# Kernel optimization log

Hardware: AMD Instinct MI355X
Metric: run time of the kernel (lower is better)

The kernel has to match this reference:

```python
import jax, jax.numpy as jnp
import numpy as np

XI_DIM = 4
LENS = jnp.array([0.5, 0.5, 1.0], dtype=jnp.float32)
NOISE_SCALE = jnp.array([0.01, 0.01], dtype=jnp.float32)
PRIOR_SCALE = jnp.array([0.25, 0.5, 0.5, 0.5], dtype=jnp.float32)
LOG2PI = float(np.log(2.0 * np.pi))
_TRIL_R, _TRIL_C = np.tril_indices(XI_DIM, k=-1)  # strict lower triangle (6 entries)


def _mlp(y, W1, b1, W2, b2, W3, b3):
    h = jax.nn.relu(y @ W1 + b1)
    h = jax.nn.relu(h @ W2 + b2)
    return h @ W3 + b3


def _forward_D(xi):
    # robot-arm forward kinematics; xi: [..., 4] -> end point D: [..., 2]
    a1 = xi[..., 1]
    a2 = a1 + xi[..., 2]
    a3 = a2 + xi[..., 3]
    px = LENS[0] * jnp.cos(a1) + LENS[1] * jnp.cos(a2) + LENS[2] * jnp.cos(a3)
    py = xi[..., 0] + LENS[0] * jnp.sin(a1) + LENS[1] * jnp.sin(a2) + LENS[2] * jnp.sin(a3)
    return jnp.stack([px, py], axis=-1)


def setup_inputs() -> dict:
    key = jax.random.key(0)
    N, P = 524288, 8
    ks = jax.random.split(key, 24)
    # observed data exactly as observed_data(): xi ~ Normal(0, prior_scale), y = f(xi)['D'] + noise
    xi_data = jax.random.normal(ks[0], (N, XI_DIM), dtype=jnp.float32) * PRIOR_SCALE
    y = _forward_D(xi_data) + NOISE_SCALE * jax.random.normal(ks[1], (N, 2), dtype=jnp.float32)
    zs = jax.random.normal(ks[2], (N, P, XI_DIM), dtype=jnp.float32)
    inp = {"y": y, "zs": zs}
    base = [("W1", (2, 20)), ("b1", (20,)), ("W2", (20, 10)), ("b2", (10,))]
    i = 3
    for pre, out_dim in (("mu", XI_DIM), ("ld", XI_DIM), ("lo", XI_DIM * (XI_DIM + 1) // 2 - XI_DIM)):
        for nm, sh in base + [("W3", (10, out_dim)), ("b3", (out_dim,))]:
            inp[f"{pre}_{nm}"] = jax.random.normal(ks[i], sh, dtype=jnp.float32) * 0.3
            i += 1
    return inp


def reference(y, zs,
              mu_W1, mu_b1, mu_W2, mu_b2, mu_W3, mu_b3,
              ld_W1, ld_b1, ld_W2, ld_b2, ld_W3, ld_b3,
              lo_W1, lo_b1, lo_W2, lo_b2, lo_W3, lo_b3):
    N, P, D = zs.shape
    q_mu = _mlp(y, mu_W1, mu_b1, mu_W2, mu_b2, mu_W3, mu_b3)                  # [N, 4]
    q_L_diag = jax.nn.softplus(_mlp(y, ld_W1, ld_b1, ld_W2, ld_b2, ld_W3, ld_b3))  # [N, 4]
    q_L_off = _mlp(y, lo_W1, lo_b1, lo_W2, lo_b2, lo_W3, lo_b3)               # [N, 6]
    # batched Cholesky factors L: [N, 4, 4]
    L = jnp.zeros((N, D, D), dtype=y.dtype)
    L = L.at[:, _TRIL_R, _TRIL_C].set(q_L_off)
    di = jnp.arange(D)
    L = L.at[:, di, di].set(q_L_diag)
    # reparameterized samples: xi = mu + L @ z, vectorized over (N, P)
    xi = q_mu[:, None, :] + jnp.einsum('nij,npj->npi', L, zs)                 # [N, P, 4]
    # prior log-prob (independent Normal(0, prior_scale)), summed over dims
    log_prior = jnp.sum(-0.5 * (xi / PRIOR_SCALE) ** 2 - jnp.log(PRIOR_SCALE) - 0.5 * LOG2PI, axis=-1)
    # likelihood: Normal(f(xi)['D'], noise_scale).log_prob(y), summed over y_dim
    Dpt = _forward_D(xi)                                                      # [N, P, 2]
    r = (y[:, None, :] - Dpt) / NOISE_SCALE
    log_lik = jnp.sum(-0.5 * r ** 2 - jnp.log(NOISE_SCALE) - 0.5 * LOG2PI, axis=-1)
    datafit = jnp.mean(log_prior + log_lik, axis=1)                           # [N]
    # MVN entropy with scale_tril L: 0.5*d*(1+log 2pi) + sum log diag(L)
    entropy = 0.5 * D * (1.0 + LOG2PI) + jnp.sum(jnp.log(q_L_diag), axis=-1)
    return jnp.mean(datafit + entropy)
```

## Files before the change

kernel.cpp:

```cpp
#include <hip/hip_runtime.h>
#include <math.h>

#define C_ALL 12.838199208f

typedef float v2 __attribute__((ext_vector_type(2)));
static __device__ __forceinline__ v2 splat(float s) { return (v2){s, s}; }
#define FMA2 __builtin_elementwise_fma
#define MAX2 __builtin_elementwise_max

struct WPtrs { const float* p[18]; };

__device__ __forceinline__ float softplus_f(float x) {
    return fmaxf(x, 0.0f) + __logf(1.0f + __expf(-fabsf(x)));
}
__device__ __forceinline__ v2 sp2(v2 x) {
    v2 r; r.x = softplus_f(x.x); r.y = softplus_f(x.y); return r;
}

template <int OD>
__device__ __forceinline__ void mlp4(const float* __restrict__ W1,
                                     const float* __restrict__ b1,
                                     const float* __restrict__ W2,
                                     const float* __restrict__ b2,
                                     const float* __restrict__ W3,
                                     const float* __restrict__ b3,
                                     v2 Y0a, v2 Y1a, v2 Y0b, v2 Y1b,
                                     v2* oa, v2* ob) {
    v2 h2a[10], h2b[10];
#pragma unroll
    for (int k = 0; k < 10; ++k) { const v2 bb = splat(b2[k]); h2a[k] = bb; h2b[k] = bb; }
#pragma unroll
    for (int j = 0; j < 20; ++j) {
        const float w0 = W1[j], w1 = W1[20 + j], bb = b1[j];
        const v2 h1a = MAX2(FMA2(Y0a, splat(w0), FMA2(Y1a, splat(w1), splat(bb))), splat(0.0f));
        const v2 h1b = MAX2(FMA2(Y0b, splat(w0), FMA2(Y1b, splat(w1), splat(bb))), splat(0.0f));
#pragma unroll
        for (int k = 0; k < 10; ++k) {
            const v2 w = splat(W2[j * 10 + k]);
            h2a[k] = FMA2(h1a, w, h2a[k]);
            h2b[k] = FMA2(h1b, w, h2b[k]);
        }
    }
#pragma unroll
    for (int k = 0; k < 10; ++k) { h2a[k] = MAX2(h2a[k], splat(0.0f)); h2b[k] = MAX2(h2b[k], splat(0.0f)); }
#pragma unroll
    for (int d = 0; d < OD; ++d) { const v2 bb = splat(b3[d]); oa[d] = bb; ob[d] = bb; }
#pragma unroll
    for (int k = 0; k < 10; ++k) {
#pragma unroll
        for (int d = 0; d < OD; ++d) {
            const v2 w = splat(W3[k * OD + d]);
            oa[d] = FMA2(h2a[k], w, oa[d]);
            ob[d] = FMA2(h2b[k], w, ob[d]);
        }
    }
}

template <int OD>
__device__ __forceinline__ void mlp1(const float* __restrict__ W1, const float* __restrict__ b1,
                                     const float* __restrict__ W2, const float* __restrict__ b2,
                                     const float* __restrict__ W3, const float* __restrict__ b3,
                                     float y0, float y1, float* out) {
    float h2[10];
#pragma unroll
    for (int k = 0; k < 10; ++k) h2[k] = b2[k];
#pragma unroll
    for (int j = 0; j < 20; ++j) {
        const float h1 = fmaxf(0.0f, fmaf(y0, W1[j], fmaf(y1, W1[20 + j], b1[j])));
#pragma unroll
        for (int k = 0; k < 10; ++k) h2[k] = fmaf(h1, W2[j * 10 + k], h2[k]);
    }
#pragma unroll
    for (int k = 0; k < 10; ++k) h2[k] = fmaxf(0.0f, h2[k]);
#pragma unroll
    for (int d = 0; d < OD; ++d) out[d] = b3[d];
#pragma unroll
    for (int k = 0; k < 10; ++k)
#pragma unroll
        for (int d = 0; d < OD; ++d) out[d] = fmaf(h2[k], W3[k * OD + d], out[d]);
}

__device__ __forceinline__ void store_params(float* __restrict__ pr, int row,
                                             float m0, float m1, float m2, float m3,
                                             float d0, float d1, float d2, float d3,
                                             float L10, float L20, float L21,
                                             float L30, float L31, float L32) {
    float4* q = reinterpret_cast<float4*>(pr + (size_t)row * 16);
    q[0] = make_float4(m0, m1, m2, m3);
    q[1] = make_float4(d0, d1, d2, d3);
    q[2] = make_float4(L10, L20, L21, L30);
    q[3] = make_float4(L31, L32, __logf(d0 * d1 * d2 * d3), 0.0f);
}

__global__ __launch_bounds__(256) void avi_params(
    const float* __restrict__ y, WPtrs wp, float* __restrict__ pr, int N) {
    const int tid = threadIdx.x;
    const int r0 = blockIdx.x * 1024 + tid;

    if (r0 + 768 < N) {
        const float2 ya = *reinterpret_cast<const float2*>(y + 2 * (size_t)(r0));
        const float2 yb = *reinterpret_cast<const float2*>(y + 2 * (size_t)(r0 + 256));
        const float2 yc = *reinterpret_cast<const float2*>(y + 2 * (size_t)(r0 + 512));
        const float2 yd = *reinterpret_cast<const float2*>(y + 2 * (size_t)(r0 + 768));
        const v2 Y0a = {ya.x, yb.x}, Y1a = {ya.y, yb.y};
        const v2 Y0b = {yc.x, yd.x}, Y1b = {yc.y, yd.y};

        v2 mua[4], mub[4], lda[4], ldb[4], loa[6], lob[6];
        mlp4<4>(wp.p[0], wp.p[1], wp.p[2], wp.p[3], wp.p[4], wp.p[5],
                Y0a, Y1a, Y0b, Y1b, mua, mub);
        mlp4<4>(wp.p[6], wp.p[7], wp.p[8], wp.p[9], wp.p[10], wp.p[11],
                Y0a, Y1a, Y0b, Y1b, lda, ldb);
        mlp4<6>(wp.p[12], wp.p[13], wp.p[14], wp.p[15], wp.p[16], wp.p[17],
                Y0a, Y1a, Y0b, Y1b, loa, lob);

        const v2 da0 = sp2(lda[0]), da1 = sp2(lda[1]), da2 = sp2(lda[2]), da3 = sp2(lda[3]);
        const v2 db0 = sp2(ldb[0]), db1 = sp2(ldb[1]), db2 = sp2(ldb[2]), db3 = sp2(ldb[3]);

        store_params(pr, r0,       mua[0].x, mua[1].x, mua[2].x, mua[3].x,
                     da0.x, da1.x, da2.x, da3.x,
                     loa[0].x, loa[1].x, loa[2].x, loa[3].x, loa[4].x, loa[5].x);
        store_params(pr, r0 + 256, mua[0].y, mua[1].y, mua[2].y, mua[3].y,
                     da0.y, da1.y, da2.y, da3.y,
                     loa[0].y, loa[1].y, loa[2].y, loa[3].y, loa[4].y, loa[5].y);
        store_params(pr, r0 + 512, mub[0].x, mub[1].x, mub[2].x, mub[3].x,
                     db0.x, db1.x, db2.x, db3.x,
                     lob[0].x, lob[1].x, lob[2].x, lob[3].x, lob[4].x, lob[5].x);
        store_params(pr, r0 + 768, mub[0].y, mub[1].y, mub[2].y, mub[3].y,
                     db0.y, db1.y, db2.y, db3.y,
                     lob[0].y, lob[1].y, lob[2].y, lob[3].y, lob[4].y, lob[5].y);
    } else {
        for (int s = 0; s < 4; ++s) {
            const int row = r0 + s * 256;
            if (row >= N) continue;
            const float2 yv = *reinterpret_cast<const float2*>(y + 2 * (size_t)row);
            float mu[4], ld[4], lo[6];
            mlp1<4>(wp.p[0], wp.p[1], wp.p[2], wp.p[3], wp.p[4], wp.p[5], yv.x, yv.y, mu);
            mlp1<4>(wp.p[6], wp.p[7], wp.p[8], wp.p[9], wp.p[10], wp.p[11], yv.x, yv.y, ld);
            mlp1<6>(wp.p[12], wp.p[13], wp.p[14], wp.p[15], wp.p[16], wp.p[17], yv.x, yv.y, lo);
            store_params(pr, row, mu[0], mu[1], mu[2], mu[3],
                         softplus_f(ld[0]), softplus_f(ld[1]), softplus_f(ld[2]), softplus_f(ld[3]),
                         lo[0], lo[1], lo[2], lo[3], lo[4], lo[5]);
        }
    }
}

__global__ __launch_bounds__(256) void avi_tail(
    const float* __restrict__ y, const float* __restrict__ zs,
    const float* __restrict__ pr, float* __restrict__ out, int N, float invN) {
    __shared__ float wsum[4];
    const int tid = threadIdx.x;
    const int n = blockIdx.x * 256 + tid;
    float rv = 0.0f;
    if (n < N) {
        const float4* pq = reinterpret_cast<const float4*>(pr + (size_t)n * 16);
        const float4 p0 = pq[0], p1 = pq[1], p2 = pq[2], p3 = pq[3];
        const float2 yv = *reinterpret_cast<const float2*>(y + 2 * (size_t)n);
        const float y0 = yv.x, y1 = yv.y;

        const float4* zp = reinterpret_cast<const float4*>(zs + (size_t)n * 32);
        float4 z[8];
#pragma unroll
        for (int p = 0; p < 8; ++p) z[p] = zp[p];
        __builtin_amdgcn_sched_barrier(0);

        const float m0 = p0.x, m1 = p0.y, m2 = p0.z, m3 = p0.w;
        const float d0 = p1.x, d1 = p1.y, d2 = p1.z, d3 = p1.w;
        const float L10 = p2.x, L20 = p2.y, L21 = p2.z, L30 = p2.w;
        const float L31 = p3.x, L32 = p3.y, slog = p3.z;

        float acc = 0.0f;
#pragma unroll
        for (int p = 0; p < 8; ++p) {
            const float xi0 = fmaf(d0, z[p].x, m0);
            const float xi1 = fmaf(d1, z[p].y, fmaf(L10, z[p].x, m1));
            const float xi2 = fmaf(d2, z[p].z, fmaf(L21, z[p].y, fmaf(L20, z[p].x, m2)));
            const float xi3 = fmaf(d3, z[p].w, fmaf(L32, z[p].z, fmaf(L31, z[p].y, fmaf(L30, z[p].x, m3))));

            const float a1 = xi1, a2 = xi1 + xi2, a3 = a2 + xi3;
            float s1, c1, s2, c2, s3, c3;
            __sincosf(a1, &s1, &c1);
            __sincosf(a2, &s2, &c2);
            __sincosf(a3, &s3, &c3);
            const float px = fmaf(0.5f, c1, fmaf(0.5f, c2, c3));
            const float py = xi0 + fmaf(0.5f, s1, fmaf(0.5f, s2, s3));

            const float q0 = xi0 * 4.0f, q1 = xi1 * 2.0f, q2 = xi2 * 2.0f, q3 = xi3 * 2.0f;
            const float pq2 = fmaf(q0, q0, fmaf(q1, q1, fmaf(q2, q2, q3 * q3)));
            const float r0 = (y0 - px) * 100.0f;
            const float r1 = (y1 - py) * 100.0f;
            acc = fmaf(-0.5f, pq2 + fmaf(r0, r0, r1 * r1), acc);
        }
        rv = fmaf(0.125f, acc, C_ALL + slog);
    }

#pragma unroll
    for (int d = 32; d > 0; d >>= 1) rv += __shfl_down(rv, d);
    if ((tid & 63) == 0) wsum[tid >> 6] = rv;
    __syncthreads();
    if (tid == 0) {
        const float s = wsum[0] + wsum[1] + wsum[2] + wsum[3];
        atomicAdd(out, s * invN);
    }
}

extern "C" void kernel_launch(void* const* d_in, const int* in_sizes, int n_in,
                              void* d_out, int out_size, void* d_ws, size_t ws_size,
                              hipStream_t stream) {
    const float* y = (const float*)d_in[0];
    const float* zs = (const float*)d_in[1];
    WPtrs wp;
    for (int i = 0; i < 18; ++i) wp.p[i] = (const float*)d_in[2 + i];
    float* out = (float*)d_out;
    float* pr = (float*)d_ws;
    const int N = in_sizes[0] / 2;

    hipMemsetAsync(out, 0, sizeof(float), stream);
    avi_params<<<(N + 1023) / 1024, 256, 0, stream>>>(y, wp, pr, N);
    avi_tail<<<(N + 255) / 256, 256, 0, stream>>>(y, zs, pr, out, N, 1.0f / (float)N);
}
```

Before: 183.5 us.

## Fuse param MLP and tail into one kernel, prefetching zs during MLP

Merges the parameter-MLP kernel and the sampling/likelihood tail kernel into a single kernel. Each thread now handles 4 rows and keeps the MLP outputs in registers instead of writing a 64-byte-per-row parameter buffer to workspace and reading it back. Half of the zs loads are issued before the MLP so their latency overlaps that compute, and the tail math is packed into 2-wide vector ops. The cost is much higher register pressure from holding 64 floats of z plus MLP state, with launch_bounds(256,2) limiting occupancy, and only N/1024 blocks in the grid.

```diff
diff --git a/kernel.cpp b/kernel.cpp
--- a/kernel.cpp
+++ b/kernel.cpp
@@ -56,6 +56,48 @@
     }
 }
 
+__device__ __forceinline__ v2 tail_pack(const v2* mu, v2 d0, v2 d1, v2 d2, v2 d3,
+                                        const v2* lo, v2 Y0, v2 Y1,
+                                        const float4* z1, const float4* z2) {
+    const v2 L10 = lo[0], L20 = lo[1], L21 = lo[2];
+    const v2 L30 = lo[3], L31 = lo[4], L32 = lo[5];
+    v2 acc = splat(0.0f);
+#pragma unroll
+    for (int p = 0; p < 8; ++p) {
+        const v2 zx = {z1[p].x, z2[p].x}, zy = {z1[p].y, z2[p].y};
+        const v2 zz = {z1[p].z, z2[p].z}, zw = {z1[p].w, z2[p].w};
+
+        const v2 xi0 = FMA2(d0, zx, mu[0]);
+        const v2 xi1 = FMA2(d1, zy, FMA2(L10, zx, mu[1]));
+        const v2 xi2 = FMA2(d2, zz, FMA2(L21, zy, FMA2(L20, zx, mu[2])));
+        const v2 xi3 = FMA2(d3, zw, FMA2(L32, zz, FMA2(L31, zy, FMA2(L30, zx, mu[3]))));
+
+        const v2 a1 = xi1, a2 = xi1 + xi2, a3 = a2 + xi3;
+        float s1x, c1x, s1y, c1y, s2x, c2x, s2y, c2y, s3x, c3x, s3y, c3y;
+        __sincosf(a1.x, &s1x, &c1x);
+        __sincosf(a1.y, &s1y, &c1y);
+        __sincosf(a2.x, &s2x, &c2x);
+        __sincosf(a2.y, &s2y, &c2y);
+        __sincosf(a3.x, &s3x, &c3x);
+        __sincosf(a3.y, &s3y, &c3y);
+        const v2 s1 = {s1x, s1y}, c1 = {c1x, c1y};
+        const v2 s2 = {s2x, s2y}, c2 = {c2x, c2y};
+        const v2 s3 = {s3x, s3y}, c3 = {c3x, c3y};
+
+        const v2 half = splat(0.5f);
+        const v2 px = FMA2(half, c1, FMA2(half, c2, c3));
+        const v2 py = xi0 + FMA2(half, s1, FMA2(half, s2, s3));
+
+        const v2 q0 = xi0 * splat(4.0f), q1 = xi1 * splat(2.0f);
+        const v2 q2 = xi2 * splat(2.0f), q3 = xi3 * splat(2.0f);
+        const v2 pq = FMA2(q0, q0, FMA2(q1, q1, FMA2(q2, q2, q3 * q3)));
+        const v2 r0 = (Y0 - px) * splat(100.0f);
+        const v2 r1 = (Y1 - py) * splat(100.0f);
+        acc = FMA2(splat(-0.5f), pq + FMA2(r0, r0, r1 * r1), acc);
+    }
+    return acc;
+}
+
 template <int OD>
 __device__ __forceinline__ void mlp1(const float* __restrict__ W1, const float* __restrict__ b1,
                                      const float* __restrict__ W2, const float* __restrict__ b2,
@@ -80,30 +122,62 @@
         for (int d = 0; d < OD; ++d) out[d] = fmaf(h2[k], W3[k * OD + d], out[d]);
 }
 
-__device__ __forceinline__ void store_params(float* __restrict__ pr, int row,
-                                             float m0, float m1, float m2, float m3,
-                                             float d0, float d1, float d2, float d3,
-                                             float L10, float L20, float L21,
-                                             float L30, float L31, float L32) {
-    float4* q = reinterpret_cast<float4*>(pr + (size_t)row * 16);
-    q[0] = make_float4(m0, m1, m2, m3);
-    q[1] = make_float4(d0, d1, d2, d3);
-    q[2] = make_float4(L10, L20, L21, L30);
-    q[3] = make_float4(L31, L32, __logf(d0 * d1 * d2 * d3), 0.0f);
-}
-
-__global__ __launch_bounds__(256) void avi_params(
-    const float* __restrict__ y, WPtrs wp, float* __restrict__ pr, int N) {
+__device__ float row_scalar(const float* __restrict__ y, const float* __restrict__ zs,
+                            const WPtrs& wp, int n) {
+    const float2 yv = *reinterpret_cast<const float2*>(y + 2 * (size_t)n);
+    const float y0 = yv.x, y1 = yv.y;
+    float mu[4], ld[4], lo[6];
+    mlp1<4>(wp.p[0], wp.p[1], wp.p[2], wp.p[3], wp.p[4], wp.p[5], y0, y1, mu);
+    mlp1<4>(wp.p[6], wp.p[7], wp.p[8], wp.p[9], wp.p[10], wp.p[11], y0, y1, ld);
+    mlp1<6>(wp.p[12], wp.p[13], wp.p[14], wp.p[15], wp.p[16], wp.p[17], y0, y1, lo);
+    const float d0 = softplus_f(ld[0]), d1 = softplus_f(ld[1]);
+    const float d2 = softplus_f(ld[2]), d3 = softplus_f(ld[3]);
+    const float slog = __logf(d0 * d1 * d2 * d3);
+    const float4* zp = reinterpret_cast<const float4*>(zs + (size_t)n * 32);
+    float acc = 0.0f;
+    for (int p = 0; p < 8; ++p) {
+        const float4 z = zp[p];
+        const float xi0 = fmaf(d0, z.x, mu[0]);
+        const float xi1 = fmaf(d1, z.y, fmaf(lo[0], z.x, mu[1]));
+        const float xi2 = fmaf(d2, z.z, fmaf(lo[2], z.y, fmaf(lo[1], z.x, mu[2])));
+        const float xi3 = fmaf(d3, z.w, fmaf(lo[5], z.z, fmaf(lo[4], z.y, fmaf(lo[3], z.x, mu[3]))));
+        const float a1 = xi1, a2 = xi1 + xi2, a3 = a2 + xi3;
+        float s1, c1, s2, c2, s3, c3;
+        __sincosf(a1, &s1, &c1); __sincosf(a2, &s2, &c2); __sincosf(a3, &s3, &c3);
+        const float px = fmaf(0.5f, c1, fmaf(0.5f, c2, c3));
+        const float py = xi0 + fmaf(0.5f, s1, fmaf(0.5f, s2, s3));
+        const float q0 = xi0 * 4.0f, q1 = xi1 * 2.0f, q2 = xi2 * 2.0f, q3 = xi3 * 2.0f;
+        const float pq = fmaf(q0, q0, fmaf(q1, q1, fmaf(q2, q2, q3 * q3)));
+        const float r0 = (y0 - px) * 100.0f;
+        const float r1 = (y1 - py) * 100.0f;
+        acc = fmaf(-0.5f, pq + fmaf(r0, r0, r1 * r1), acc);
+    }
+    return fmaf(0.125f, acc, C_ALL + slog);
+}
+
+__global__ __launch_bounds__(256, 2) void avi_kernel(
+    const float* __restrict__ y, const float* __restrict__ zs, WPtrs wp,
+    float* __restrict__ out, int N, float invN) {
+    __shared__ float wsum[4];
+
     const int tid = threadIdx.x;
     const int r0 = blockIdx.x * 1024 + tid;
-
+    float rv = 0.0f;
     if (r0 + 768 < N) {
-        const float2 ya = *reinterpret_cast<const float2*>(y + 2 * (size_t)(r0));
-        const float2 yb = *reinterpret_cast<const float2*>(y + 2 * (size_t)(r0 + 256));
-        const float2 yc = *reinterpret_cast<const float2*>(y + 2 * (size_t)(r0 + 512));
-        const float2 yd = *reinterpret_cast<const float2*>(y + 2 * (size_t)(r0 + 768));
-        const v2 Y0a = {ya.x, yb.x}, Y1a = {ya.y, yb.y};
-        const v2 Y0b = {yc.x, yd.x}, Y1b = {yc.y, yd.y};
+        const float2 ya1 = *reinterpret_cast<const float2*>(y + 2 * (size_t)r0);
+        const float2 ya2 = *reinterpret_cast<const float2*>(y + 2 * (size_t)(r0 + 256));
+        const float2 yb1 = *reinterpret_cast<const float2*>(y + 2 * (size_t)(r0 + 512));
+        const float2 yb2 = *reinterpret_cast<const float2*>(y + 2 * (size_t)(r0 + 768));
+
+        const float4* zp_a1 = reinterpret_cast<const float4*>(zs + (size_t)r0 * 32);
+        const float4* zp_a2 = reinterpret_cast<const float4*>(zs + (size_t)(r0 + 256) * 32);
+        float4 za1[8], za2[8];
+#pragma unroll
+        for (int p = 0; p < 8; ++p) { za1[p] = zp_a1[p]; za2[p] = zp_a2[p]; }
+        __builtin_amdgcn_sched_barrier(0);
+
+        const v2 Y0a = {ya1.x, ya2.x}, Y1a = {ya1.y, ya2.y};
+        const v2 Y0b = {yb1.x, yb2.x}, Y1b = {yb1.y, yb2.y};
 
         v2 mua[4], mub[4], lda[4], ldb[4], loa[6], lob[6];
         mlp4<4>(wp.p[0], wp.p[1], wp.p[2], wp.p[3], wp.p[4], wp.p[5],
@@ -113,84 +187,30 @@
         mlp4<6>(wp.p[12], wp.p[13], wp.p[14], wp.p[15], wp.p[16], wp.p[17],
                 Y0a, Y1a, Y0b, Y1b, loa, lob);
 
+        const float4* zp_b1 = reinterpret_cast<const float4*>(zs + (size_t)(r0 + 512) * 32);
+        const float4* zp_b2 = reinterpret_cast<const float4*>(zs + (size_t)(r0 + 768) * 32);
+        float4 zb1[8], zb2[8];
+#pragma unroll
+        for (int p = 0; p < 8; ++p) { zb1[p] = zp_b1[p]; zb2[p] = zp_b2[p]; }
+        __builtin_amdgcn_sched_barrier(0);
+
         const v2 da0 = sp2(lda[0]), da1 = sp2(lda[1]), da2 = sp2(lda[2]), da3 = sp2(lda[3]);
         const v2 db0 = sp2(ldb[0]), db1 = sp2(ldb[1]), db2 = sp2(ldb[2]), db3 = sp2(ldb[3]);
-
-        store_params(pr, r0,       mua[0].x, mua[1].x, mua[2].x, mua[3].x,
-                     da0.x, da1.x, da2.x, da3.x,
-                     loa[0].x, loa[1].x, loa[2].x, loa[3].x, loa[4].x, loa[5].x);
-        store_params(pr, r0 + 256, mua[0].y, mua[1].y, mua[2].y, mua[3].y,
-                     da0.y, da1.y, da2.y, da3.y,
-                     loa[0].y, loa[1].y, loa[2].y, loa[3].y, loa[4].y, loa[5].y);
-        store_params(pr, r0 + 512, mub[0].x, mub[1].x, mub[2].x, mub[3].x,
-                     db0.x, db1.x, db2.x, db3.x,
-                     lob[0].x, lob[1].x, lob[2].x, lob[3].x, lob[4].x, lob[5].x);
-        store_params(pr, r0 + 768, mub[0].y, mub[1].y, mub[2].y, mub[3].y,
-                     db0.y, db1.y, db2.y, db3.y,
-                     lob[0].y, lob[1].y, lob[2].y, lob[3].y, lob[4].y, lob[5].y);
+        const v2 prodA = da0 * da1 * da2 * da3;
+        const v2 prodB = db0 * db1 * db2 * db3;
+
+        const v2 accA = tail_pack(mua, da0, da1, da2, da3, loa, Y0a, Y1a, za1, za2);
+        const v2 accB = tail_pack(mub, db0, db1, db2, db3, lob, Y0b, Y1b, zb1, zb2);
+
+        rv = fmaf(0.125f, accA.x, C_ALL + __logf(prodA.x))
+           + fmaf(0.125f, accA.y, C_ALL + __logf(prodA.y))
+           + fmaf(0.125f, accB.x, C_ALL + __logf(prodB.x))
+           + fmaf(0.125f, accB.y, C_ALL + __logf(prodB.y));
     } else {
         for (int s = 0; s < 4; ++s) {
             const int row = r0 + s * 256;
-            if (row >= N) continue;
-            const float2 yv = *reinterpret_cast<const float2*>(y + 2 * (size_t)row);
-            float mu[4], ld[4], lo[6];
-            mlp1<4>(wp.p[0], wp.p[1], wp.p[2], wp.p[3], wp.p[4], wp.p[5], yv.x, yv.y, mu);
-            mlp1<4>(wp.p[6], wp.p[7], wp.p[8], wp.p[9], wp.p[10], wp.p[11], yv.x, yv.y, ld);
-            mlp1<6>(wp.p[12], wp.p[13], wp.p[14], wp.p[15], wp.p[16], wp.p[17], yv.x, yv.y, lo);
-            store_params(pr, row, mu[0], mu[1], mu[2], mu[3],
-                         softplus_f(ld[0]), softplus_f(ld[1]), softplus_f(ld[2]), softplus_f(ld[3]),
-                         lo[0], lo[1], lo[2], lo[3], lo[4], lo[5]);
+            if (row < N) rv += row_scalar(y, zs, wp, row);
         }
-    }
-}
-
-__global__ __launch_bounds__(256) void avi_tail(
-    const float* __restrict__ y, const float* __restrict__ zs,
-    const float* __restrict__ pr, float* __restrict__ out, int N, float invN) {
-    __shared__ float wsum[4];
-    const int tid = threadIdx.x;
-    const int n = blockIdx.x * 256 + tid;
-    float rv = 0.0f;
-    if (n < N) {
-        const float4* pq = reinterpret_cast<const float4*>(pr + (size_t)n * 16);
-        const float4 p0 = pq[0], p1 = pq[1], p2 = pq[2], p3 = pq[3];
-        const float2 yv = *reinterpret_cast<const float2*>(y + 2 * (size_t)n);
-        const float y0 = yv.x, y1 = yv.y;
-
-        const float4* zp = reinterpret_cast<const float4*>(zs + (size_t)n * 32);
-        float4 z[8];
-#pragma unroll
-        for (int p = 0; p < 8; ++p) z[p] = zp[p];
-        __builtin_amdgcn_sched_barrier(0);
-
-        const float m0 = p0.x, m1 = p0.y, m2 = p0.z, m3 = p0.w;
-        const float d0 = p1.x, d1 = p1.y, d2 = p1.z, d3 = p1.w;
-        const float L10 = p2.x, L20 = p2.y, L21 = p2.z, L30 = p2.w;
-        const float L31 = p3.x, L32 = p3.y, slog = p3.z;
-
-        float acc = 0.0f;
-#pragma unroll
-        for (int p = 0; p < 8; ++p) {
-            const float xi0 = fmaf(d0, z[p].x, m0);
-            const float xi1 = fmaf(d1, z[p].y, fmaf(L10, z[p].x, m1));
-            const float xi2 = fmaf(d2, z[p].z, fmaf(L21, z[p].y, fmaf(L20, z[p].x, m2)));
-            const float xi3 = fmaf(d3, z[p].w, fmaf(L32, z[p].z, fmaf(L31, z[p].y, fmaf(L30, z[p].x, m3))));
-
-            const float a1 = xi1, a2 = xi1 + xi2, a3 = a2 + xi3;
-            float s1, c1, s2, c2, s3, c3;
-            __sincosf(a1, &s1, &c1);
-            __sincosf(a2, &s2, &c2);
-            __sincosf(a3, &s3, &c3);
-            const float px = fmaf(0.5f, c1, fmaf(0.5f, c2, c3));
-            const float py = xi0 + fmaf(0.5f, s1, fmaf(0.5f, s2, s3));
-
-            const float q0 = xi0 * 4.0f, q1 = xi1 * 2.0f, q2 = xi2 * 2.0f, q3 = xi3 * 2.0f;
-            const float pq2 = fmaf(q0, q0, fmaf(q1, q1, fmaf(q2, q2, q3 * q3)));
-            const float r0 = (y0 - px) * 100.0f;
-            const float r1 = (y1 - py) * 100.0f;
-            acc = fmaf(-0.5f, pq2 + fmaf(r0, r0, r1 * r1), acc);
-        }
-        rv = fmaf(0.125f, acc, C_ALL + slog);
     }
 
 #pragma unroll
@@ -211,10 +231,9 @@
     WPtrs wp;
     for (int i = 0; i < 18; ++i) wp.p[i] = (const float*)d_in[2 + i];
     float* out = (float*)d_out;
-    float* pr = (float*)d_ws;
     const int N = in_sizes[0] / 2;
 
     hipMemsetAsync(out, 0, sizeof(float), stream);
-    avi_params<<<(N + 1023) / 1024, 256, 0, stream>>>(y, wp, pr, N);
-    avi_tail<<<(N + 255) / 256, 256, 0, stream>>>(y, zs, pr, out, N, 1.0f / (float)N);
-}
+    const int blocks = (N + 1023) / 1024;
+    avi_kernel<<<blocks, 256, 0, stream>>>(y, zs, wp, out, N, 1.0f / (float)N);
+}
```

Result: faster. 159.3 us (-13.2%).
